# Kernel tuning notes

Hardware: AMD Instinct MI355X
Metric: run time of the kernel (lower is better)

The kernel has to match this reference:

```python
import jax, jax.numpy as jnp
import numpy as np

GRID_SIZE = 8
SPLINE_ORDER = 3
GRID_LO, GRID_HI = -1.0, 1.0
EPS = 1e-5  # InstanceNorm2d default eps
C = 16
K = GRID_SIZE + SPLINE_ORDER  # number of B-spline basis channels per input channel


def make_grid():
    h = (GRID_HI - GRID_LO) / GRID_SIZE
    # extended knot vector, length grid_size + 2*spline_order + 1
    return jnp.arange(-SPLINE_ORDER, GRID_SIZE + SPLINE_ORDER + 1, dtype=jnp.float32) * h + GRID_LO


def bspline_bases(x, grid):
    # x: [B,C,H,W] -> bases: [B,C,H,W,K] via Cox-de Boor recursion
    xu = x[..., None]
    bases = ((xu >= grid[:-1]) & (xu < grid[1:])).astype(x.dtype)
    for k in range(1, SPLINE_ORDER + 1):
        left = grid[:-(k + 1)]
        right = grid[k:-1]
        delta = jnp.where(right == left, jnp.ones_like(right), right - left)
        bases = ((xu - left) / delta) * bases[..., :-1] + \
                ((grid[k + 1:] - xu) / (grid[k + 1:] - grid[1:-k])) * bases[..., 1:]
    return bases


def conv2d(x, w):
    # NCHW conv, stride 1, padding 1 (kernel 3x3), bias=False as in KANConv2DLayer
    return jax.lax.conv_general_dilated(
        x, w, window_strides=(1, 1), padding=[(1, 1), (1, 1)],
        dimension_numbers=('NCHW', 'OIHW', 'NCHW'))


def instance_norm(x):
    # nn.InstanceNorm2d(affine=False): normalize over H,W per (N,C)
    m = jnp.mean(x, axis=(2, 3), keepdims=True)
    v = jnp.var(x, axis=(2, 3), keepdims=True)
    return (x - m) * jax.lax.rsqrt(v + EPS)


def prelu(x, a):
    return jnp.where(x >= 0, x, a * x)


def kan_conv_layer(x, base_w, spline_w, prelu_a, grid):
    base_out = conv2d(jax.nn.silu(x), base_w)
    b = bspline_bases(x, grid)                      # [B,C,H,W,K]
    B, Cx, H, W, Kx = b.shape
    b = jnp.moveaxis(b, -1, 2).reshape(B, Cx * Kx, H, W)
    spline_out = conv2d(b, spline_w)
    return prelu(instance_norm(base_out + spline_out), prelu_a)


def setup_inputs() -> dict:
    key = jax.random.key(0)
    ks = jax.random.split(key, 5)
    s = 0.05
    return {
        'x': jax.random.normal(ks[0], (4, C, 512, 512), jnp.float32),
        'base_w1': jax.random.normal(ks[1], (C, C, 3, 3), jnp.float32) * s,
        'spline_w1': jax.random.normal(ks[2], (C, C * K, 3, 3), jnp.float32) * s,
        'prelu_a1': jnp.float32(0.25),
        'base_w2': jax.random.normal(ks[3], (C, C, 3, 3), jnp.float32) * s,
        'spline_w2': jax.random.normal(ks[4], (C, C * K, 3, 3), jnp.float32) * s,
        'prelu_a2': jnp.float32(0.25),
    }


def reference(x, base_w1, spline_w1, prelu_a1, base_w2, spline_w2, prelu_a2):
    grid = make_grid()
    y = kan_conv_layer(x, base_w1, spline_w1, prelu_a1, grid)
    y = kan_conv_layer(y, base_w2, spline_w2, prelu_a2, grid)
    return jax.nn.sigmoid(y)
```

## Files before the change

### kernel.cpp

```cpp
#include <hip/hip_runtime.h>
#include <cstddef>
#include <cstdint>

#define HW    512
#define CCH   16
#define HTILE 18
#define NPIX  324
#define NPIXS 326
#define NSLOT 12

typedef _Float16 f16x8 __attribute__((ext_vector_type(8)));
typedef float    f32x4 __attribute__((ext_vector_type(4)));

__device__ __forceinline__ float h2f(ushort u) {
    _Float16 h = __builtin_bit_cast(_Float16, u);
    return (float)h;
}
__device__ __forceinline__ ushort f2h(float f) {
    _Float16 h = (_Float16)f;
    return __builtin_bit_cast(ushort, h);
}
__device__ __forceinline__ uint pack2h(float a, float b) {
    return (uint)f2h(a) | ((uint)f2h(b) << 16);
}

__device__ __forceinline__ void derived12(float x, uint* u) {
    float si = x / (1.0f + __expf(-x));
    float t  = fmaf(x, 4.0f, 7.0f);
    t = fminf(fmaxf(t, -1.0f), 15.0f);
    float ft = floorf(t);
    int   ci = (int)ft;
    float uu = t - ft;
    float um = 1.0f - uu;
    float u2 = uu * uu, m2 = um * um;
    float u3 = u2 * uu, m3 = m2 * um;
    const float c16 = 0.16666667f, c23 = 0.66666667f;
    float w0 = u3 * c16;
    float w3 = m3 * c16;
    float w2 = fmaf(0.5f, u3, c23 - u2);
    float w1 = fmaf(0.5f, m3, c23 - m2);
    uint64_t P = (uint64_t)f2h(w3)
               | ((uint64_t)f2h(w2) << 16)
               | ((uint64_t)f2h(w1) << 32)
               | ((uint64_t)f2h(w0) << 48);
    int s = 16 * ci - 48;
    int d = s >> 6;
    int e = s & 63;
    uint64_t Q = P << e;
    uint64_t R = (P >> (63 - e)) >> 1;
    uint64_t O0 = (d == 0) ? Q : (d == -1) ? R : 0ull;
    uint64_t O1 = (d == 1) ? Q : (d ==  0) ? R : 0ull;
    uint64_t O2 = (d == 2) ? Q : (d ==  1) ? R : 0ull;
    O2 = (O2 & 0x0000ffffffffffffull) | ((uint64_t)f2h(si) << 48);
    u[0] = (uint)O0; u[1] = (uint)(O0 >> 32);
    u[2] = (uint)O1; u[3] = (uint)(O1 >> 32);
    u[4] = (uint)O2; u[5] = (uint)(O2 >> 32);
}

__global__ void __launch_bounds__(64) prep_w(
    const float* __restrict__ bw1, const float* __restrict__ sw1,
    const float* __restrict__ bw2, const float* __restrict__ sw2,
    uint4* __restrict__ wtab1, uint4* __restrict__ wtab2,
    float* __restrict__ part1, float* __restrict__ part2)
{
    const int s    = blockIdx.x;
    const int lane = threadIdx.x;
    const float* bw; const float* sw; uint4* wt;
    if (blockIdx.y == 0) { bw = bw1; sw = sw1; wt = wtab1; }
    else                 { bw = bw2; sw = sw2; wt = wtab2; }

    if (s == 0) {
        float* p = (blockIdx.y == 0) ? part1 : part2;
        p[lane] = 0.0f;
        p[64 + lane] = 0.0f;
    }

    const int co = lane & 15, q = lane >> 4;
    const int chunk = s / 27, sl = s - chunk * 27;
    uint u[4];
#pragma unroll
    for (int jj = 0; jj < 4; ++jj) {
        float w[2];
#pragma unroll
        for (int h = 0; h < 2; ++h) {
            int j   = jj * 2 + h;
            int kl  = 32 * sl + 8 * q + j;
            int tap = kl / 96;
            int r   = kl - tap * 96;
            int ci  = r / 12;
            int kv  = r - ci * 12;
            int cin = chunk * 8 + ci;
            w[h] = (kv == 11) ? bw[(co * 16 + cin) * 9 + tap]
                              : sw[(co * 176 + cin * 11 + kv) * 9 + tap];
        }
        u[jj] = pack2h(w[0], w[1]);
    }
    wt[s * 64 + lane] = make_uint4(u[0], u[1], u[2], u[3]);
}

template<bool IN_H, bool OUT_H, bool NORM_IN>
__global__ __launch_bounds__(256, 2) void conv_mfma(
    const void* __restrict__ in_v,
    const uint4* __restrict__ wtab,
    void* __restrict__ out_v,
    const float* __restrict__ part_in,
    const float* __restrict__ a_in,
    float* __restrict__ part_out)
{
    __shared__ uint4 dt16[NSLOT * NPIXS];
    __shared__ float sn[32];

    const int tid  = threadIdx.x;
    const int lane = tid & 63;
    const int wv   = tid >> 6;
    const int m    = lane & 15;
    const int q    = lane >> 4;
    const int bx0  = blockIdx.x * 16;
    const int by0  = blockIdx.y * 16;
    const int b    = blockIdx.z;

    const float*  inf = (const float*)in_v;
    const ushort* inh = (const ushort*)in_v;

    float pa = 0.0f;
    if (NORM_IN) {
        pa = *a_in;
        if (tid < 32) {
            int ci = tid >> 1;
            float s  = part_in[(b * CCH + ci) * 2];
            float qq = part_in[(b * CCH + ci) * 2 + 1];
            const float inv = 1.0f / 262144.0f;
            float mv  = s * inv;
            float var = qq * inv - mv * mv;
            sn[tid] = (tid & 1) ? rsqrtf(var + 1e-5f) : mv;
        }
    }

    f32x4 acc[4];
#pragma unroll
    for (int t = 0; t < 4; ++t) acc[t] = f32x4{0.f, 0.f, 0.f, 0.f};

#pragma unroll 1
    for (int chunk = 0; chunk < 2; ++chunk) {
        __syncthreads();

        float v0[6], v1[6];
        uint  bofs[6], cps[6];
        bool  live[6];
#pragma unroll
        for (int k = 0; k < 6; ++k) {
            int it  = tid + k * 256;
            bool lv = (it < NPIX * 4);
            int cp  = it & 3;
            int pix = it >> 2;
            if (!lv) pix = 0;
            int py  = pix / 18;
            int px  = pix - py * 18;
            int gy  = by0 + py - 1;
            int gx  = bx0 + px - 1;
            bool ok = lv && ((unsigned)gy < (unsigned)HW)
                         && ((unsigned)gx < (unsigned)HW);
            live[k] = lv;
            cps[k]  = (uint)cp;
            bofs[k] = (uint)(cp * 3 * NPIXS + pix);
            float a = -1.0e9f, c = -1.0e9f;
            if (ok) {
                size_t base = ((size_t)(b * CCH + chunk * 8 + cp * 2) << 18)
                            + ((size_t)gy << 9) + gx;
                if (IN_H) { a = h2f(inh[base]); c = h2f(inh[base + (1u << 18)]); }
                else      { a = inf[base];      c = inf[base + (1u << 18)]; }
            }
            v0[k] = a; v1[k] = c;
        }

        uint4 wf[27];
#pragma unroll
        for (int s = 0; s < 27; ++s) wf[s] = wtab[(chunk * 27 + s) * 64 + lane];

#pragma unroll
        for (int k = 0; k < 6; ++k) {
            if (live[k]) {
                float a0 = v0[k], c0 = v1[k];
                if (NORM_IN) {
                    int ci2 = (chunk * 8 + (int)cps[k] * 2) * 2;
                    a0 = (a0 - sn[ci2])     * sn[ci2 + 1];
                    a0 = (a0 >= 0.f) ? a0 : pa * a0;
                    c0 = (c0 - sn[ci2 + 2]) * sn[ci2 + 3];
                    c0 = (c0 >= 0.f) ? c0 : pa * c0;
                }
                uint uA[6], uB[6];
                derived12(a0, uA);
                derived12(c0, uB);
                uint bo = bofs[k];
                dt16[bo]             = make_uint4(uA[0], uA[1], uA[2], uA[3]);
                dt16[bo + NPIXS]     = make_uint4(uA[4], uA[5], uB[0], uB[1]);
                dt16[bo + 2 * NPIXS] = make_uint4(uB[2], uB[3], uB[4], uB[5]);
            }
        }
        __syncthreads();

        const uint pixbase = (uint)(wv * 72 + m);
#pragma unroll
        for (int j = 0; j < 3; ++j) {
            const uint slotoff = (uint)((j * 4 + q) * NPIXS) + pixbase;
#pragma unroll
            for (int tdx = 0; tdx < 3; ++tdx) {
                f16x8 brow[6];
#pragma unroll
                for (int r6 = 0; r6 < 6; ++r6)
                    brow[r6] = *reinterpret_cast<const f16x8*>(
                        &dt16[slotoff + (uint)(r6 * HTILE + tdx)]);
#pragma unroll
                for (int tdy = 0; tdy < 3; ++tdy) {
                    const int s = (tdy * 3 + tdx) * 3 + j;
#pragma unroll
                    for (int t = 0; t < 4; ++t) {
                        acc[t] = __builtin_amdgcn_mfma_f32_16x16x32_f16(
                            __builtin_bit_cast(f16x8, wf[s]), brow[t + tdy],
                            acc[t], 0, 0, 0);
                    }
                }
            }
        }
    }

#pragma unroll
    for (int t = 0; t < 4; ++t) {
        int oy = by0 + wv * 4 + t;
#pragma unroll
        for (int r = 0; r < 4; ++r) {
            int co = q * 4 + r;
            size_t idx = ((size_t)(b * CCH + co) << 18) + ((size_t)oy << 9) + (bx0 + m);
            if (OUT_H) ((ushort*)out_v)[idx] = f2h(acc[t][r]);
            else       ((float*)out_v)[idx]  = acc[t][r];
        }
    }

    float s4[4], q4[4];
#pragma unroll
    for (int r = 0; r < 4; ++r) {
        s4[r] = acc[0][r] + acc[1][r] + acc[2][r] + acc[3][r];
        q4[r] = fmaf(acc[0][r], acc[0][r],
                fmaf(acc[1][r], acc[1][r],
                fmaf(acc[2][r], acc[2][r], acc[3][r] * acc[3][r])));
    }
#pragma unroll
    for (int off = 8; off > 0; off >>= 1) {
#pragma unroll
        for (int r = 0; r < 4; ++r) {
            s4[r] += __shfl_xor(s4[r], off);
            q4[r] += __shfl_xor(q4[r], off);
        }
    }
    __syncthreads();
    float* scr = (float*)dt16;
    if (m == 0) {
#pragma unroll
        for (int r = 0; r < 4; ++r) {
            scr[(wv * 16 + q * 4 + r) * 2 + 0] = s4[r];
            scr[(wv * 16 + q * 4 + r) * 2 + 1] = q4[r];
        }
    }
    __syncthreads();
    if (tid < 32) {
        int co = tid >> 1, which = tid & 1;
        float v = scr[(0 * 16 + co) * 2 + which] + scr[(1 * 16 + co) * 2 + which]
                + scr[(2 * 16 + co) * 2 + which] + scr[(3 * 16 + co) * 2 + which];
        atomicAdd(&part_out[(size_t)(b * CCH + co) * 2 + which], v);
    }
}

__global__ void __launch_bounds__(256) final_sigmoid(
    float* __restrict__ out, const float* __restrict__ part,
    const float* __restrict__ a_ptr)
{
    const float a = *a_ptr;
    const int i4 = blockIdx.x * 256 + threadIdx.x;
    const int bc = blockIdx.x >> 8;
    const float inv = 1.0f / 262144.0f;
    const float s  = part[bc * 2];
    const float qq = part[bc * 2 + 1];
    const float mm = s * inv;
    const float rr = rsqrtf(qq * inv - mm * mm + 1e-5f);
    float4 v = reinterpret_cast<float4*>(out)[i4];
    float t;
    t = (v.x - mm) * rr; t = (t >= 0.f) ? t : a * t; v.x = 1.0f / (1.0f + __expf(-t));
    t = (v.y - mm) * rr; t = (t >= 0.f) ? t : a * t; v.y = 1.0f / (1.0f + __expf(-t));
    t = (v.z - mm) * rr; t = (t >= 0.f) ? t : a * t; v.z = 1.0f / (1.0f + __expf(-t));
    t = (v.w - mm) * rr; t = (t >= 0.f) ? t : a * t; v.w = 1.0f / (1.0f + __expf(-t));
    reinterpret_cast<float4*>(out)[i4] = v;
}

extern "C" void kernel_launch(void* const* d_in, const int* in_sizes, int n_in,
                              void* d_out, int out_size, void* d_ws, size_t ws_size,
                              hipStream_t stream)
{
    const float* x        = (const float*)d_in[0];
    const float* base_w1  = (const float*)d_in[1];
    const float* spline_w1= (const float*)d_in[2];
    const float* prelu_a1 = (const float*)d_in[3];
    const float* base_w2  = (const float*)d_in[4];
    const float* spline_w2= (const float*)d_in[5];
    const float* prelu_a2 = (const float*)d_in[6];
    float* out_f = (float*)d_out;
    char*  wsb   = (char*)d_ws;

    ushort* z1h    = (ushort*)wsb;
    uint4*  wtab1  = (uint4*)(wsb + 33554432);
    uint4*  wtab2  = (uint4*)(wsb + 33609728);
    float*  part1  = (float*)(wsb + 33665024);
    float*  part2  = (float*)(wsb + 33665536);

    dim3 cgrid(HW / 16, HW / 16, 4);
    dim3 cblk(256);

    prep_w<<<dim3(54, 2), 64, 0, stream>>>(base_w1, spline_w1, base_w2, spline_w2,
                                           wtab1, wtab2, part1, part2);

    conv_mfma<false, true, false><<<cgrid, cblk, 0, stream>>>(
        x, wtab1, z1h, nullptr, nullptr, part1);

    conv_mfma<true, false, true><<<cgrid, cblk, 0, stream>>>(
        z1h, wtab2, out_f, part1, prelu_a1, part2);

    final_sigmoid<<<16384, cblk, 0, stream>>>(out_f, part2, prelu_a2);
}
```

Measured before the change: 360.1 us.

## Prefetch second channel chunk's global loads during first chunk's MFMA loop

Restructures the two-chunk loop into explicit stages so the global loads for chunk 1 are issued before the MFMA accumulation of chunk 0, hiding memory latency behind compute. Per-thread pixel index and bounds math is hoisted out of the chunk loop and computed once. This costs extra registers (12 more floats held across the MFMA phase), which could raise VGPR pressure and lower occupancy.

```diff
diff --git a/kernel.cpp b/kernel.cpp
--- a/kernel.cpp
+++ b/kernel.cpp
@@ -136,53 +136,49 @@
         }
     }
 
-    f32x4 acc[4];
-#pragma unroll
-    for (int t = 0; t < 4; ++t) acc[t] = f32x4{0.f, 0.f, 0.f, 0.f};
-
-#pragma unroll 1
-    for (int chunk = 0; chunk < 2; ++chunk) {
-        __syncthreads();
-
-        float v0[6], v1[6];
-        uint  bofs[6], cps[6];
-        bool  live[6];
+    uint goff[6], bofs6[6];
+    bool ok6[6], live6[6];
+#pragma unroll
+    for (int k = 0; k < 6; ++k) {
+        int it  = tid + k * 256;
+        bool lv = (it < NPIX * 4);
+        int cp  = it & 3;
+        int pix = it >> 2;
+        if (!lv) pix = 0;
+        int py  = pix / 18;
+        int px  = pix - py * 18;
+        int gy  = by0 + py - 1;
+        int gx  = bx0 + px - 1;
+        live6[k] = lv;
+        ok6[k]   = lv && ((unsigned)gy < (unsigned)HW)
+                      && ((unsigned)gx < (unsigned)HW);
+        goff[k]  = ((uint)gy << 9) + (uint)gx;
+        bofs6[k] = (uint)(cp * 3 * NPIXS + pix);
+    }
+
+    auto loads = [&](int chunk, float* V) {
 #pragma unroll
         for (int k = 0; k < 6; ++k) {
-            int it  = tid + k * 256;
-            bool lv = (it < NPIX * 4);
-            int cp  = it & 3;
-            int pix = it >> 2;
-            if (!lv) pix = 0;
-            int py  = pix / 18;
-            int px  = pix - py * 18;
-            int gy  = by0 + py - 1;
-            int gx  = bx0 + px - 1;
-            bool ok = lv && ((unsigned)gy < (unsigned)HW)
-                         && ((unsigned)gx < (unsigned)HW);
-            live[k] = lv;
-            cps[k]  = (uint)cp;
-            bofs[k] = (uint)(cp * 3 * NPIXS + pix);
+            int cp = (tid + k * 256) & 3;
             float a = -1.0e9f, c = -1.0e9f;
-            if (ok) {
+            if (ok6[k]) {
                 size_t base = ((size_t)(b * CCH + chunk * 8 + cp * 2) << 18)
-                            + ((size_t)gy << 9) + gx;
+                            + goff[k];
                 if (IN_H) { a = h2f(inh[base]); c = h2f(inh[base + (1u << 18)]); }
                 else      { a = inf[base];      c = inf[base + (1u << 18)]; }
             }
-            v0[k] = a; v1[k] = c;
-        }
-
-        uint4 wf[27];
-#pragma unroll
-        for (int s = 0; s < 27; ++s) wf[s] = wtab[(chunk * 27 + s) * 64 + lane];
-
+            V[2 * k] = a; V[2 * k + 1] = c;
+        }
+    };
+
+    auto derive_write = [&](int chunk, const float* V) {
 #pragma unroll
         for (int k = 0; k < 6; ++k) {
-            if (live[k]) {
-                float a0 = v0[k], c0 = v1[k];
+            if (live6[k]) {
+                int cp = (tid + k * 256) & 3;
+                float a0 = V[2 * k], c0 = V[2 * k + 1];
                 if (NORM_IN) {
-                    int ci2 = (chunk * 8 + (int)cps[k] * 2) * 2;
+                    int ci2 = (chunk * 8 + cp * 2) * 2;
                     a0 = (a0 - sn[ci2])     * sn[ci2 + 1];
                     a0 = (a0 >= 0.f) ? a0 : pa * a0;
                     c0 = (c0 - sn[ci2 + 2]) * sn[ci2 + 3];
@@ -191,14 +187,22 @@
                 uint uA[6], uB[6];
                 derived12(a0, uA);
                 derived12(c0, uB);
-                uint bo = bofs[k];
+                uint bo = bofs6[k];
                 dt16[bo]             = make_uint4(uA[0], uA[1], uA[2], uA[3]);
                 dt16[bo + NPIXS]     = make_uint4(uA[4], uA[5], uB[0], uB[1]);
                 dt16[bo + 2 * NPIXS] = make_uint4(uB[2], uB[3], uB[4], uB[5]);
             }
         }
-        __syncthreads();
-
+    };
+
+    f32x4 acc[4];
+#pragma unroll
+    for (int t = 0; t < 4; ++t) acc[t] = f32x4{0.f, 0.f, 0.f, 0.f};
+
+    auto krun = [&](int chunk) {
+        uint4 wf[27];
+#pragma unroll
+        for (int s = 0; s < 27; ++s) wf[s] = wtab[(chunk * 27 + s) * 64 + lane];
         const uint pixbase = (uint)(wv * 72 + m);
 #pragma unroll
         for (int j = 0; j < 3; ++j) {
@@ -222,7 +226,19 @@
                 }
             }
         }
-    }
+    };
+
+    float va[12], vb[12];
+    loads(0, va);
+    __syncthreads();
+    derive_write(0, va);
+    __syncthreads();
+    loads(1, vb);
+    krun(0);
+    __syncthreads();
+    derive_write(1, vb);
+    __syncthreads();
+    krun(1);
 
 #pragma unroll
     for (int t = 0; t < 4; ++t) {
```

Result: slower. 398.4 us (+10.6%).
